# Performance work log

Hardware: AMD Instinct MI355X
Metric: run time of the kernel (lower is better)

## Reference

```python
import jax, jax.numpy as jnp
import numpy as np

B, CIN, H, W = 2, 8, 224, 224
P, S, K, WIN = 10, 5, 7, 3      # patchsize, stride, k neighbours, window radius = 15 // stride
E, F = 8, 64                    # embedding out-channels, cnn hidden features
N1 = (H - P) // S + 1
N2 = (W - P) // S + 1
N = N1 * N2                     # patches per image (43*43 = 1849)


def _conv(x, w, b):
    y = jax.lax.conv_general_dilated(x, w, (1, 1), 'SAME',
                                     dimension_numbers=('NCHW', 'OIHW', 'NCHW'))
    return y + b[None, :, None, None]


def _cnn3(x, w1, b1, w2, b2, w3, b3):
    # conv-relu, conv-relu, conv (depth=3, bn disabled)
    h = jax.nn.relu(_conv(x, w1, b1))
    h = jax.nn.relu(_conv(h, w2, b2))
    return _conv(h, w3, b3)


def _patches(x):
    # x: [B,C,H,W] -> [B, N, C*P*P] (im2col with stride S)
    ri = jnp.arange(N1)[:, None] * S + jnp.arange(P)[None, :]   # [N1,P]
    ci = jnp.arange(N2)[:, None] * S + jnp.arange(P)[None, :]   # [N2,P]
    p = x[:, :, ri, :][..., ci]            # [B,C,N1,P,N2,P]
    p = p.transpose(0, 2, 4, 1, 3, 5)      # [B,N1,N2,C,P,P]
    return p.reshape(x.shape[0], N, -1)


def _candidates():
    q1, q2 = jnp.meshgrid(jnp.arange(N1), jnp.arange(N2), indexing='ij')
    off = jnp.arange(-WIN, WIN + 1)
    c1 = jnp.clip(q1[..., None, None] + off[:, None], 0, N1 - 1)   # [N1,N2,7,7]
    c2 = jnp.clip(q2[..., None, None] + off[None, :], 0, N2 - 1)
    return (c1 * N2 + c2).reshape(N, -1)   # [N, m], m=49


def _fold(pats, C):
    # pats: [B,N,C*P*P] -> [B,C,H,W], overlap-add then normalize by counts
    pats = pats.reshape(B, N, C, P, P).transpose(0, 2, 1, 3, 4).reshape(B, C, -1)
    rr = jnp.arange(N1)[:, None] * S + jnp.arange(P)[None, :]
    cc = jnp.arange(N2)[:, None] * S + jnp.arange(P)[None, :]
    R = jnp.broadcast_to(rr[:, None, :, None], (N1, N2, P, P)).reshape(-1)
    Cc = jnp.broadcast_to(cc[None, :, None, :], (N1, N2, P, P)).reshape(-1)
    out = jnp.zeros((B, C, H, W), pats.dtype).at[:, :, R, Cc].add(pats)
    cnt = jnp.zeros((H, W), pats.dtype).at[R, Cc].add(1.0)
    return out / jnp.maximum(cnt, 1.0)


def setup_inputs() -> dict:
    key = jax.random.key(0)
    ks = jax.random.split(key, 8)
    sd = 0.05
    d = {"x": jax.random.normal(ks[0], (B, CIN, H, W), jnp.float32)}
    # embedding cnn: CIN->F->F->E
    d["w1e"] = jax.random.normal(ks[1], (F, CIN, 3, 3), jnp.float32) * sd
    d["b1e"] = jnp.zeros((F,), jnp.float32)
    d["w2e"] = jax.random.normal(ks[2], (F, F, 3, 3), jnp.float32) * sd
    d["b2e"] = jnp.zeros((F,), jnp.float32)
    d["w3e"] = jax.random.normal(ks[3], (E, F, 3, 3), jnp.float32) * sd
    d["b3e"] = jnp.zeros((E,), jnp.float32)
    # temperature cnn: CIN->F->F->1
    d["w1t"] = jax.random.normal(ks[4], (F, CIN, 3, 3), jnp.float32) * sd
    d["b1t"] = jnp.zeros((F,), jnp.float32)
    d["w2t"] = jax.random.normal(ks[5], (F, F, 3, 3), jnp.float32) * sd
    d["b2t"] = jnp.zeros((F,), jnp.float32)
    d["w3t"] = jax.random.normal(ks[6], (1, F, 3, 3), jnp.float32) * sd
    d["b3t"] = jnp.zeros((1,), jnp.float32)
    return d


def reference(x, w1e, b1e, w2e, b2e, w3e, b3e, w1t, b1t, w2t, b2t, w3t, b3t):
    xe = _cnn3(x, w1e, b1e, w2e, b2e, w3e, b3e)           # [B,E,H,W] patch embedding
    log_temp = _cnn3(x, w1t, b1t, w2t, b2t, w3t, b3t)     # [B,1,H,W] log temperature

    pe = _patches(xe)                                     # [B,N,E*P*P]
    yp = _patches(x)                                      # [B,N,CIN*P*P]
    lt = _patches(log_temp).mean(-1)                      # [B,N] per-patch log temp
    idx = _candidates()                                   # [N,m]

    # negative squared euclidean distance, gathered at window candidates
    sq = jnp.sum(pe * pe, -1)                             # [B,N]
    G = jnp.einsum('bnd,bmd->bnm', pe, pe)                # [B,N,N] patch Gram
    Dfull = -(sq[:, :, None] + sq[:, None, :] - 2.0 * G)
    Dc = Dfull[:, jnp.arange(N)[:, None], idx]            # [B,N,m]

    self_mask = (idx == jnp.arange(N)[:, None])[None]     # exclude_self=True
    logits = Dc * jnp.exp(-lt)[..., None]                 # temperature-scaled
    logits = jnp.where(self_mask, -1e9, logits)

    # continuous (neural) k-nearest-neighbour weights
    ws, cur = [], logits
    for _ in range(K):
        w = jax.nn.softmax(cur, axis=-1)
        ws.append(w)
        cur = cur + jnp.log1p(-jnp.minimum(w, 1.0 - 1e-6))
    Wk = jnp.stack(ws, axis=-1)                           # [B,N,m,K]

    yg = yp[:, idx]                                       # [B,N,m,dy] gathered neighbour patches
    nb = jnp.einsum('bnmk,bnmd->kbnd', Wk, yg)            # [K,B,N,dy]
    vols = [_fold(nb[j], CIN) for j in range(K)]
    return jnp.concatenate([x] + vols, axis=1)            # [B,(K+1)*CIN,H,W]
```

## Files before the change

kernel.cpp:

```cpp
#include <hip/hip_runtime.h>
#include <math.h>

namespace {
constexpr int B_ = 2, CIN = 8, H_ = 224, W_ = 224;
constexpr int K_ = 7;
constexpr int F_ = 64, E_ = 8;
constexpr int N1 = 43, N2 = 43, N_ = N1 * N2;
constexpr int M_ = 49;
constexpr int D_ = 800;
constexpr int HW = H_ * W_;

constexpr size_t FHW = (size_t)B_ * F_ * HW;
constexpr size_t OFF_H1E = 0;
constexpr size_t OFF_H1T = OFF_H1E + FHW;
constexpr size_t OFF_H2E = OFF_H1T + FHW;
constexpr size_t OFF_H2T = OFF_H2E + FHW;
constexpr size_t OFF_WK  = 0;
constexpr size_t OFF_XE  = OFF_H2T + FHW;
constexpr size_t OFF_LTM = OFF_XE + (size_t)B_ * E_ * HW;
constexpr size_t OFF_PE  = OFF_LTM + (size_t)B_ * HW;
constexpr size_t OFF_LT  = OFF_PE + (size_t)B_ * N_ * D_;
constexpr size_t OFF_SQ  = OFF_LT + (size_t)B_ * N_;
constexpr int WPREP_N = 294912;
constexpr int WPREP1_N = 12288;
constexpr int WPREP3_N = 9216;
constexpr int WPREP_TOT = WPREP_N + WPREP1_N + 2 * WPREP3_N;

__device__ __forceinline__ int clampi(int v, int lo, int hi) {
  return min(max(v, lo), hi);
}

__device__ __forceinline__ int xcd_swz(int x, int nwg) {
  int xcd = x & 7, idx = x >> 3;
  int q = nwg >> 3, r = nwg & 7;
  int base = (xcd < r) ? xcd * (q + 1) : r * (q + 1) + (xcd - r) * q;
  return base + idx;
}

typedef __attribute__((ext_vector_type(8))) short short8;
typedef __attribute__((ext_vector_type(4))) float float4v;
typedef __attribute__((ext_vector_type(4))) unsigned short ushort4v;
}

__global__ __launch_bounds__(256) void wprep_k(
    const float* __restrict__ w_e, const float* __restrict__ w_t,
    const float* __restrict__ w1e, const float* __restrict__ w1t,
    const float* __restrict__ w3e, const float* __restrict__ w3t,
    unsigned short* __restrict__ whi, unsigned short* __restrict__ wlo,
    unsigned short* __restrict__ whi1, unsigned short* __restrict__ wlo1,
    unsigned short* __restrict__ whi3, unsigned short* __restrict__ wlo3) {
  int t = blockIdx.x * 256 + threadIdx.x;
  if (t >= WPREP_TOT) return;
  float v;
  unsigned short* dh;
  unsigned short* dl;
  int di;
  if (t < WPREP_N) {
    int j = t & 7;
    int lane = (t >> 3) & 63;
    int wv = (t >> 9) & 3;
    int t2 = t >> 11;
    int idx = t2 % 9;
    int t3 = t2 / 9;
    int kcb = t3 & 1;
    int br = t3 >> 1;
    const float* wgt = br ? w_t : w_e;
    int co = wv * 16 + (lane & 15);
    int ci = kcb * 32 + 8 * (lane >> 4) + j;
    v = wgt[((size_t)co * 64 + ci) * 9 + idx];
    dh = whi; dl = wlo; di = t;
  } else if (t < WPREP_N + WPREP1_N) {
    int t1 = t - WPREP_N;
    int j = t1 & 7;
    int lane = (t1 >> 3) & 63;
    int wv = (t1 >> 9) & 3;
    int t2 = t1 >> 11;
    int ky = t2 % 3;
    int br = t2 / 3;
    const float* wgt = br ? w1t : w1e;
    int co = wv * 16 + (lane & 15);
    int kx = lane >> 4;
    int ci = j;
    v = (kx < 3) ? wgt[(((size_t)co * 8 + ci) * 3 + ky) * 3 + kx] : 0.f;
    dh = whi1; dl = wlo1; di = t1;
  } else {
    int t3v = t - WPREP_N - WPREP1_N;
    int set = t3v / WPREP3_N;
    int rem = t3v - set * WPREP3_N;
    int j = rem & 7;
    int lane = (rem >> 3) & 63;
    int t2 = rem >> 9;
    int idx = t2 % 9;
    int kcb = t2 / 9;
    int co = lane & 15;
    int ci = kcb * 32 + 8 * (lane >> 4) + j;
    if (set == 0)
      v = (co < 8) ? w3e[((size_t)co * 64 + ci) * 9 + idx] : 0.f;
    else
      v = (co == 0) ? w3t[(size_t)ci * 9 + idx] : 0.f;
    dh = whi3; dl = wlo3; di = t3v;
  }
  unsigned u = __float_as_uint(v);
  unsigned short hi = (unsigned short)(u >> 16);
  float rem = v - __uint_as_float(u & 0xffff0000u);
  unsigned short lo = (unsigned short)(__float_as_uint(rem) >> 16);
  dh[di] = hi;
  dl[di] = lo;
}

__global__ __launch_bounds__(256) void conv1_k(
    const float* __restrict__ x,
    const unsigned short* __restrict__ whi1, const unsigned short* __restrict__ wlo1,
    const float* __restrict__ b_e, float* __restrict__ o_e,
    const float* __restrict__ b_t, float* __restrict__ o_t) {
  const int tile = blockIdx.x;
  const int b = blockIdx.z & 1;
  const int br = blockIdx.z >> 1;
  const float* bias = br ? b_t : b_e;
  float* out = br ? o_t : o_e;

  const int th0 = (tile / 14) * 16, tw0 = (tile % 14) * 16;
  const int tid = threadIdx.x;
  const int wv = tid >> 6, lane = tid & 63;
  const int q = lane >> 4, n = lane & 15;

  __shared__ unsigned short sT[342 * 20];

  const float* xB = x + (size_t)b * CIN * HW;
#pragma unroll
  for (int it = 0; it < 2; ++it) {
    int s = tid + 256 * it;
    if (s < 342) {
      int lr = s / 19, lc = s - lr * 19;
      int gh = th0 + lr - 1, gw = tw0 + lc - 1;
      short8 h8, l8;
#pragma unroll
      for (int ci = 0; ci < 8; ++ci) { h8[ci] = 0; l8[ci] = 0; }
      if (lc < 18 && gh >= 0 && gh < H_ && gw >= 0 && gw < W_) {
        const float* xp = xB + (size_t)gh * W_ + gw;
#pragma unroll
        for (int ci = 0; ci < 8; ++ci) {
          float v = xp[(size_t)ci * HW];
          unsigned u = __float_as_uint(v);
          float rem = v - __uint_as_float(u & 0xffff0000u);
          h8[ci] = (short)(u >> 16);
          l8[ci] = (short)(__float_as_uint(rem) >> 16);
        }
      }
      *(short8*)&sT[s * 20] = h8;
      *(short8*)&sT[s * 20 + 8] = l8;
    }
  }

  const short8* wh8 = (const short8*)whi1;
  const short8* wl8 = (const short8*)wlo1;
  short8 Ah[3], Al[3];
#pragma unroll
  for (int ky = 0; ky < 3; ++ky) {
    int ab = ((br * 3 + ky) * 4 + wv) * 64 + lane;
    Ah[ky] = wh8[ab];
    Al[ky] = wl8[ab];
  }

  float4v acc[16];
#pragma unroll
  for (int pr = 0; pr < 16; ++pr) acc[pr] = (float4v)0.f;

  __syncthreads();

#pragma unroll
  for (int r = 0; r < 18; ++r) {
    const unsigned short* p = &sT[(r * 19 + n + q) * 20];
    short8 Bh = *(const short8*)p;
    short8 Bl = *(const short8*)(p + 8);
#pragma unroll
    for (int ky = 0; ky < 3; ++ky) {
      const int pr = r - ky;
      if (pr >= 0 && pr < 16) {
        acc[pr] = __builtin_amdgcn_mfma_f32_16x16x32_bf16(Ah[ky], Bh, acc[pr], 0, 0, 0);
        acc[pr] = __builtin_amdgcn_mfma_f32_16x16x32_bf16(Al[ky], Bh, acc[pr], 0, 0, 0);
        acc[pr] = __builtin_amdgcn_mfma_f32_16x16x32_bf16(Ah[ky], Bl, acc[pr], 0, 0, 0);
      }
    }
  }

  float4v bv = *(const float4v*)&bias[wv * 16 + 4 * q];
#pragma unroll
  for (int pr = 0; pr < 16; ++pr) {
    float4v v;
#pragma unroll
    for (int r = 0; r < 4; ++r) v[r] = fmaxf(acc[pr][r] + bv[r], 0.f);
    *(float4v*)&out[(((size_t)b * H_ + th0 + pr) * W_ + tw0 + n) * 64 + wv * 16 + 4 * q] = v;
  }
}

__global__ __launch_bounds__(256) void conv2_mfma_k(
    const float* __restrict__ in_e, const float* __restrict__ in_t,
    const unsigned short* __restrict__ whi, const unsigned short* __restrict__ wlo,
    const float* __restrict__ b_e, const float* __restrict__ b_t,
    unsigned short* __restrict__ ehi, unsigned short* __restrict__ elo,
    unsigned short* __restrict__ thi, unsigned short* __restrict__ tlo) {
  constexpr int NLD = 21;
  const int tile = blockIdx.x;
  const int b = blockIdx.z & 1;
  const int br = blockIdx.z >> 1;
  const float* in = br ? in_t : in_e;
  const float* bias = br ? b_t : b_e;
  unsigned short* ohi = br ? thi : ehi;
  unsigned short* olo = br ? tlo : elo;

  const int th0 = (tile / 14) * 16, tw0 = (tile % 14) * 16;
  const int tid = threadIdx.x;
  const int wv = tid >> 6, lane = tid & 63;
  const int q = lane >> 4, n = lane & 15;

  __shared__ unsigned short sT[18 * 18 * 72];
  unsigned* sT32 = (unsigned*)sT;

  float4v acc[16];
#pragma unroll
  for (int pr = 0; pr < 16; ++pr) acc[pr] = (float4v)0.f;

  const float* inB = in + (size_t)b * HW * 64;
  const short8* whi8 = (const short8*)whi;
  const short8* wlo8 = (const short8*)wlo;

  int po[NLD];
  unsigned okm = 0;
#pragma unroll
  for (int j = 0; j < NLD; ++j) {
    int s = tid + 256 * j;
    int sp = s >> 4, cp = s & 15;
    int lr = sp / 18, lc = sp - lr * 18;
    int gh = th0 + lr - 1, gw = tw0 + lc - 1;
    bool ok = (s < 5184) && gh >= 0 && gh < H_ && gw >= 0 && gw < W_;
    po[j] = ok ? (gh * W_ + gw) * 64 + 2 * cp : 0;
    if (ok) okm |= (1u << j);
  }

  for (int kcb = 0; kcb < 2; ++kcb) {
    float2 stg[NLD];
#pragma unroll
    for (int j = 0; j < NLD; ++j)
      stg[j] = *(const float2*)&inB[(size_t)po[j] + kcb * 32];

    __syncthreads();
#pragma unroll
    for (int j = 0; j < NLD; ++j) {
      int s = tid + 256 * j;
      if (s < 5184) {
        int sp = s >> 4, cp = s & 15;
        bool ok = (okm >> j) & 1;
        float vx = ok ? stg[j].x : 0.f;
        float vy = ok ? stg[j].y : 0.f;
        unsigned u0 = __float_as_uint(vx), u1 = __float_as_uint(vy);
        float r0 = vx - __uint_as_float(u0 & 0xffff0000u);
        float r1 = vy - __uint_as_float(u1 & 0xffff0000u);
        unsigned l0 = __float_as_uint(r0) >> 16, l1 = __float_as_uint(r1) >> 16;
        sT32[sp * 36 + cp] = (u0 >> 16) | ((u1 >> 16) << 16);
        sT32[sp * 36 + 16 + cp] = l0 | (l1 << 16);
      }
    }
    __syncthreads();

    short8 Ah[9], Al[9];
    const int abase = (((br * 2 + kcb) * 9) * 4 + wv) * 64 + lane;
#pragma unroll
    for (int idx = 0; idx < 9; ++idx) {
      Ah[idx] = whi8[abase + idx * 256];
      Al[idx] = wlo8[abase + idx * 256];
    }

#pragma unroll
    for (int r = 0; r < 18; ++r) {
      short8 Bh[3], Bl[3];
#pragma unroll
      for (int kx = 0; kx < 3; ++kx) {
        const unsigned short* p = &sT[(r * 18 + n + kx) * 72 + 8 * q];
        Bh[kx] = *(const short8*)p;
        Bl[kx] = *(const short8*)(p + 32);
      }
#pragma unroll
      for (int ky = 0; ky < 3; ++ky) {
        const int pr = r - ky;
        if (pr >= 0 && pr < 16) {
#pragma unroll
          for (int kx = 0; kx < 3; ++kx) {
            const int idx = ky * 3 + kx;
            acc[pr] = __builtin_amdgcn_mfma_f32_16x16x32_bf16(Ah[idx], Bh[kx], acc[pr], 0, 0, 0);
            acc[pr] = __builtin_amdgcn_mfma_f32_16x16x32_bf16(Al[idx], Bh[kx], acc[pr], 0, 0, 0);
            acc[pr] = __builtin_amdgcn_mfma_f32_16x16x32_bf16(Ah[idx], Bl[kx], acc[pr], 0, 0, 0);
          }
        }
      }
    }
  }

  float4v bv = *(const float4v*)&bias[wv * 16 + 4 * q];
  unsigned short* sHi = (unsigned short*)sT;
  unsigned short* sLo = sHi + 128 * 68;
  __syncthreads();
#pragma unroll
  for (int hf = 0; hf < 2; ++hf) {
#pragma unroll
    for (int pr8 = 0; pr8 < 8; ++pr8) {
      int pr = hf * 8 + pr8;
      int px = pr8 * 16 + n;
      ushort4v hv, lv;
#pragma unroll
      for (int r = 0; r < 4; ++r) {
        float v = fmaxf(acc[pr][r] + bv[r], 0.f);
        unsigned u = __float_as_uint(v);
        float rem = v - __uint_as_float(u & 0xffff0000u);
        hv[r] = (unsigned short)(u >> 16);
        lv[r] = (unsigned short)(__float_as_uint(rem) >> 16);
      }
      *(ushort4v*)&sHi[px * 68 + wv * 16 + 4 * q] = hv;
      *(ushort4v*)&sLo[px * 68 + wv * 16 + 4 * q] = lv;
    }
    __syncthreads();
#pragma unroll
    for (int i = 0; i < 4; ++i) {
      int f = tid + 256 * i;
      int px = f >> 3, c8 = f & 7;
      int h = th0 + hf * 8 + (px >> 4), w = tw0 + (px & 15);
      size_t o = ((size_t)(b * H_ + h) * W_ + w) * 64 + c8 * 8;
      *(short8*)&ohi[o] = *(const short8*)&sHi[px * 68 + c8 * 8];
      *(short8*)&olo[o] = *(const short8*)&sLo[px * 68 + c8 * 8];
    }
    __syncthreads();
  }
}

__global__ __launch_bounds__(256) void conv3_mfma_k(
    const unsigned short* __restrict__ h2ehi, const unsigned short* __restrict__ h2elo,
    const unsigned short* __restrict__ h2thi, const unsigned short* __restrict__ h2tlo,
    const unsigned short* __restrict__ whi3, const unsigned short* __restrict__ wlo3,
    const float* __restrict__ b3e, const float* __restrict__ b3t,
    float* __restrict__ xe, float* __restrict__ ltm) {
  constexpr int NLD = 12;
  const int tile = blockIdx.x;
  const int b = blockIdx.z & 1;
  const int br = blockIdx.z >> 1;
  const unsigned short* ihi = (br ? h2thi : h2ehi) + (size_t)b * HW * 64;
  const unsigned short* ilo = (br ? h2tlo : h2elo) + (size_t)b * HW * 64;

  const int th0 = (tile / 14) * 8, tw0 = (tile % 14) * 16;
  const int tid = threadIdx.x;
  const int wv = tid >> 6, lane = tid & 63;
  const int q = lane >> 4, n = lane & 15;

  __shared__ unsigned short sT[180 * 72];
  unsigned* sT32 = (unsigned*)sT;

  int po[NLD];
  unsigned okm = 0;
#pragma unroll
  for (int j = 0; j < NLD; ++j) {
    int s = tid + 256 * j;
    int sp = s >> 4, cp = s & 15;
    int lr = sp / 18, lc = sp - lr * 18;
    int gh = th0 + lr - 1, gw = tw0 + lc - 1;
    bool ok = (s < 2880) && gh >= 0 && gh < H_ && gw >= 0 && gw < W_;
    po[j] = ok ? (gh * W_ + gw) * 64 + 2 * cp : 0;
    if (ok) okm |= (1u << j);
  }

  const short8* wh8 = (const short8*)whi3;
  const short8* wl8 = (const short8*)wlo3;
  const int brBase = br * 1152;

  float4v acc[2];
  acc[0] = (float4v)0.f;
  acc[1] = (float4v)0.f;

  for (int kcb = 0; kcb < 2; ++kcb) {
    unsigned sgh[NLD], sgl[NLD];
#pragma unroll
    for (int j = 0; j < NLD; ++j) {
      sgh[j] = *(const unsigned*)&ihi[(size_t)po[j] + kcb * 32];
      sgl[j] = *(const unsigned*)&ilo[(size_t)po[j] + kcb * 32];
    }
    __syncthreads();
#pragma unroll
    for (int j = 0; j < NLD; ++j) {
      int s = tid + 256 * j;
      if (s < 2880) {
        int sp = s >> 4, cp = s & 15;
        bool ok = (okm >> j) & 1;
        sT32[sp * 36 + cp] = ok ? sgh[j] : 0u;
        sT32[sp * 36 + 16 + cp] = ok ? sgl[j] : 0u;
      }
    }
    __syncthreads();

    short8 Ah[9], Al[9];
#pragma unroll
    for (int idx = 0; idx < 9; ++idx) {
      int fe = brBase + (kcb * 9 + idx) * 64 + lane;
      Ah[idx] = wh8[fe];
      Al[idx] = wl8[fe];
    }

#pragma unroll
    for (int r = 0; r < 4; ++r) {
      const int rr = 2 * wv + r;
      short8 Bh[3], Bl[3];
#pragma unroll
      for (int kx = 0; kx < 3; ++kx) {
        const unsigned short* p = &sT[(rr * 18 + n + kx) * 72 + 8 * q];
        Bh[kx] = *(const short8*)p;
        Bl[kx] = *(const short8*)(p + 32);
      }
#pragma unroll
      for (int ky = 0; ky < 3; ++ky) {
        const int pl = r - ky;
        if (pl >= 0 && pl < 2) {
#pragma unroll
          for (int kx = 0; kx < 3; ++kx) {
            const int idx = ky * 3 + kx;
            acc[pl] = __builtin_amdgcn_mfma_f32_16x16x32_bf16(Ah[idx], Bh[kx], acc[pl], 0, 0, 0);
            acc[pl] = __builtin_amdgcn_mfma_f32_16x16x32_bf16(Al[idx], Bh[kx], acc[pl], 0, 0, 0);
            acc[pl] = __builtin_amdgcn_mfma_f32_16x16x32_bf16(Ah[idx], Bl[kx], acc[pl], 0, 0, 0);
          }
        }
      }
    }
  }

  if (br == 0) {
    if (q < 2) {
      float4v bv = *(const float4v*)&b3e[4 * q];
#pragma unroll
      for (int pl = 0; pl < 2; ++pl) {
        int h = th0 + 2 * wv + pl;
#pragma unroll
        for (int r = 0; r < 4; ++r)
          xe[((size_t)(b * 8 + 4 * q + r) * H_ + h) * W_ + tw0 + n] = acc[pl][r] + bv[r];
      }
    }
  } else {
    if (q == 0) {
      float bt = b3t[0];
#pragma unroll
      for (int pl = 0; pl < 2; ++pl) {
        int h = th0 + 2 * wv + pl;
        ltm[(size_t)b * HW + h * W_ + tw0 + n] = acc[pl][0] + bt;
      }
    }
  }
}

__global__ __launch_bounds__(256) void prep_k(const float* __restrict__ xe,
                                              const float* __restrict__ ltm,
                                              float* __restrict__ pe,
                                              float* __restrict__ lt,
                                              float* __restrict__ sq) {
  const int n = blockIdx.x, b = blockIdx.y;
  const int tid = threadIdx.x;
  const int wv = tid >> 6, lane = tid & 63;
  const int q1 = n / N2, q2 = n % N2;
  const int r0 = q1 * 5, c0 = q2 * 5;

  float s = 0.f;
  float* peR = pe + ((size_t)b * N_ + n) * D_;
#pragma unroll
  for (int j = 0; j < 4; ++j) {
    int d = tid + 256 * j;
    if (d < D_) {
      int c = d / 100;
      int rr = (d / 10) % 10;
      int cc = d % 10;
      size_t si = ((size_t)(b * 8 + c) * H_ + r0 + rr) * W_ + c0 + cc;
      float ve = xe[si];
      peR[d] = ve;
      s += ve * ve;
    }
  }
  float t = 0.f;
  if (tid < 100) t = ltm[(size_t)b * HW + (r0 + tid / 10) * W_ + c0 + tid % 10];

#pragma unroll
  for (int off = 32; off > 0; off >>= 1) {
    s += __shfl_xor(s, off);
    t += __shfl_xor(t, off);
  }
  __shared__ float rs[4], rt[4];
  if (lane == 0) { rs[wv] = s; rt[wv] = t; }
  __syncthreads();
  if (tid == 0) {
    sq[b * N_ + n] = rs[0] + rs[1] + rs[2] + rs[3];
    lt[b * N_ + n] = (rt[0] + rt[1] + rt[2] + rt[3]) * 0.01f;
  }
}

__global__ __launch_bounds__(256) void attn_w_k(const float* __restrict__ pe,
                                                const float* __restrict__ lt,
                                                const float* __restrict__ sq,
                                                float* __restrict__ wk) {
  const int wv = threadIdx.x >> 6, lane = threadIdx.x & 63;
  const int ng = xcd_swz(blockIdx.x, (N_ + 3) / 4);
  const int n = ng * 4 + wv;
  if (n >= N_) return;
  const int b = blockIdx.y;
  const int q1 = n / N2, q2 = n % N2;

  const float* peB = pe + (size_t)b * N_ * D_;
  const float* qrow = peB + (size_t)n * D_;
  float q[13];
#pragma unroll
  for (int t = 0; t < 13; ++t) {
    int s = t * 64 + lane;
    q[t] = (s < D_) ? qrow[s] : 0.f;
  }

  const float sqn = sq[b * N_ + n];
  const float itemp = expf(-lt[b * N_ + n]);
  float gm = -INFINITY;

  for (int o1 = 0; o1 < 7; ++o1) {
    int c1 = clampi(q1 + o1 - 3, 0, N1 - 1);
    const float* rowb = peB + (size_t)(c1 * N2) * D_;
#pragma unroll
    for (int o2 = 0; o2 < 7; ++o2) {
      int c2 = clampi(q2 + o2 - 3, 0, N2 - 1);
      int cn = c1 * N2 + c2;
      const float* crow = rowb + (size_t)c2 * D_;
      float a = 0.f;
#pragma unroll
      for (int t = 0; t < 13; ++t) {
        float v;
        if (t < 12) v = crow[t * 64 + lane];
        else v = (lane < 32) ? crow[768 + lane] : 0.f;
        a += q[t] * v;
      }
#pragma unroll
      for (int off = 32; off > 0; off >>= 1) a += __shfl_xor(a, off);
      float Dv = -(sqn + sq[b * N_ + cn] - 2.f * a);
      float lg = (cn == n) ? -1e9f : Dv * itemp;
      const int m = o1 * 7 + o2;
      gm = (lane == m) ? lg : gm;
    }
  }

  float cur = (lane < M_) ? gm : -INFINITY;
  float* wrow = wk + (size_t)(b * N_ + n) * (M_ * K_);
#pragma unroll
  for (int k = 0; k < K_; ++k) {
    float mx = cur;
#pragma unroll
    for (int off = 32; off > 0; off >>= 1) mx = fmaxf(mx, __shfl_xor(mx, off));
    float e = (lane < M_) ? expf(cur - mx) : 0.f;
    float ssum = e;
#pragma unroll
    for (int off = 32; off > 0; off >>= 1) ssum += __shfl_xor(ssum, off);
    float w = e / ssum;
    if (lane < M_) wrow[lane * K_ + k] = w;
    cur += log1pf(-fminf(w, 1.f - 1e-6f));
  }
}

__global__ __launch_bounds__(256) void foldpv_k(const float* __restrict__ x,
                                                const float* __restrict__ wk,
                                                float* __restrict__ out) {
  int i = blockIdx.x * 256 + threadIdx.x;
  if (i >= B_ * HW) return;
  const int w = i % W_;
  const int h = (i / W_) % H_;
  const int b = i / HW;
  const int c0 = blockIdx.z * 4;

  const float* xB = x + (size_t)b * CIN * HW;
  const int pix = h * W_ + w;
  float* outB = out + (size_t)b * 64 * HW + pix;

#pragma unroll
  for (int c = 0; c < 4; ++c)
    outB[(size_t)(c0 + c) * HW] = xB[(size_t)(c0 + c) * HW + pix];

  const int q1lo = max(0, (h - 5) / 5), q1hi = min(N1 - 1, h / 5);
  const int q2lo = max(0, (w - 5) / 5), q2hi = min(N2 - 1, w / 5);

  float acc[4][7];
#pragma unroll
  for (int c = 0; c < 4; ++c)
#pragma unroll
    for (int k = 0; k < 7; ++k) acc[c][k] = 0.f;

  int cnt = 0;
  for (int q1 = q1lo; q1 <= q1hi; ++q1) {
    const int ib = h - 5 * q1;
    for (int q2 = q2lo; q2 <= q2hi; ++q2) {
      ++cnt;
      const int jb = w - 5 * q2;
      const int n = q1 * N2 + q2;
      const float* wrow = wk + (size_t)(b * N_ + n) * (M_ * K_);
#pragma unroll
      for (int o1 = 0; o1 < 7; ++o1) {
        const int c1 = clampi(q1 + o1 - 3, 0, N1 - 1);
        const int row = c1 * 5 + ib;
#pragma unroll
        for (int o2 = 0; o2 < 7; ++o2) {
          const int c2 = clampi(q2 + o2 - 3, 0, N2 - 1);
          const int col = c2 * 5 + jb;
          const float* xp = xB + (size_t)c0 * HW + (size_t)row * W_ + col;
          float xv[4];
#pragma unroll
          for (int c = 0; c < 4; ++c) xv[c] = xp[(size_t)c * HW];
          const float* wp = wrow + (o1 * 7 + o2) * 7;
          float wm[7];
#pragma unroll
          for (int k = 0; k < 7; ++k) wm[k] = wp[k];
#pragma unroll
          for (int c = 0; c < 4; ++c)
#pragma unroll
            for (int k = 0; k < 7; ++k) acc[c][k] += wm[k] * xv[c];
        }
      }
    }
  }

  const float inv = (cnt > 0) ? 1.f / (float)cnt : 0.f;
#pragma unroll
  for (int k = 0; k < 7; ++k)
#pragma unroll
    for (int c = 0; c < 4; ++c)
      outB[(size_t)(8 + k * 8 + c0 + c) * HW] = acc[c][k] * inv;
}

extern "C" void kernel_launch(void* const* d_in, const int* in_sizes, int n_in,
                              void* d_out, int out_size, void* d_ws,
                              size_t ws_size, hipStream_t stream) {
  const float* x   = (const float*)d_in[0];
  const float* w1e = (const float*)d_in[1];
  const float* b1e = (const float*)d_in[2];
  const float* w2e = (const float*)d_in[3];
  const float* b2e = (const float*)d_in[4];
  const float* w3e = (const float*)d_in[5];
  const float* b3e = (const float*)d_in[6];
  const float* w1t = (const float*)d_in[7];
  const float* b1t = (const float*)d_in[8];
  const float* w2t = (const float*)d_in[9];
  const float* b2t = (const float*)d_in[10];
  const float* w3t = (const float*)d_in[11];
  const float* b3t = (const float*)d_in[12];

  float* ws  = (float*)d_ws;
  float* out = (float*)d_out;

  float* h1e = ws + OFF_H1E;
  float* h1t = ws + OFF_H1T;
  unsigned short* h2ehi = (unsigned short*)(ws + OFF_H2E);
  unsigned short* h2elo = h2ehi + (size_t)B_ * HW * 64;
  unsigned short* h2thi = (unsigned short*)(ws + OFF_H2T);
  unsigned short* h2tlo = h2thi + (size_t)B_ * HW * 64;
  float* wkb = ws + OFF_WK;
  float* xe  = ws + OFF_XE;
  float* ltm = ws + OFF_LTM;
  float* pe  = ws + OFF_PE;
  float* lt  = ws + OFF_LT;
  float* sqv = ws + OFF_SQ;
  unsigned short* whi  = (unsigned short*)(ws + OFF_XE);
  unsigned short* wlo  = whi + WPREP_N;
  unsigned short* whi1 = wlo + WPREP_N;
  unsigned short* wlo1 = whi1 + WPREP1_N;
  unsigned short* whi3 = (unsigned short*)(ws + OFF_PE);
  unsigned short* wlo3 = whi3 + 2 * WPREP3_N;

  wprep_k<<<(WPREP_TOT + 255) / 256, 256, 0, stream>>>(
      w2e, w2t, w1e, w1t, w3e, w3t, whi, wlo, whi1, wlo1, whi3, wlo3);
  conv1_k<<<dim3(196, 1, 4), 256, 0, stream>>>(x, whi1, wlo1, b1e, h1e, b1t, h1t);
  conv2_mfma_k<<<dim3(196, 1, 4), 256, 0, stream>>>(h1e, h1t, whi, wlo, b2e, b2t,
                                                    h2ehi, h2elo, h2thi, h2tlo);
  conv3_mfma_k<<<dim3(392, 1, 4), 256, 0, stream>>>(h2ehi, h2elo, h2thi, h2tlo,
                                                    whi3, wlo3, b3e, b3t, xe, ltm);
  prep_k<<<dim3(N_, B_), 256, 0, stream>>>(xe, ltm, pe, lt, sqv);
  attn_w_k<<<dim3((N_ + 3) / 4, B_), 256, 0, stream>>>(pe, lt, sqv, wkb);
  foldpv_k<<<dim3((B_ * HW + 255) / 256, 1, 2), 256, 0, stream>>>(x, wkb, out);
}
```

Measured before the change: 332.8 us.

## Tile foldpv into 16x16 blocks with LDS-staged weights and channel-last input

Adds a kernel that transposes the input x into a channel-last copy, so the fold kernel can fetch 4 channels with one vector load. The fold kernel now works on 16x16 pixel tiles with XCD-swizzled block ids. It stages the neighbour weights for all patches covering the tile into shared memory, padded from 7 to 8 entries so they can be read as vectors. This replaces redundant per-thread global loads of weights and strided channel loads, at the cost of an extra transpose kernel, about 39KB of LDS per block, and reuse of the h1t workspace region.

Result: faster. 301.4 us (-9.4%).

```diff
diff --git a/kernel.cpp b/kernel.cpp
--- a/kernel.cpp
+++ b/kernel.cpp
@@ -16,6 +16,7 @@
 constexpr size_t OFF_H2E = OFF_H1T + FHW;
 constexpr size_t OFF_H2T = OFF_H2E + FHW;
 constexpr size_t OFF_WK  = 0;
+constexpr size_t OFF_XCL = OFF_H1T;
 constexpr size_t OFF_XE  = OFF_H2T + FHW;
 constexpr size_t OFF_LTM = OFF_XE + (size_t)B_ * E_ * HW;
 constexpr size_t OFF_PE  = OFF_LTM + (size_t)B_ * HW;
@@ -39,6 +40,7 @@
 
 typedef __attribute__((ext_vector_type(8))) short short8;
 typedef __attribute__((ext_vector_type(4))) float float4v;
+typedef __attribute__((ext_vector_type(2))) float float2v;
 typedef __attribute__((ext_vector_type(4))) unsigned short ushort4v;
 }
 
@@ -451,6 +453,21 @@
   }
 }
 
+__global__ __launch_bounds__(256) void xcl_k(const float* __restrict__ x,
+                                             float* __restrict__ xcl) {
+  int i = blockIdx.x * 256 + threadIdx.x;
+  if (i >= B_ * HW) return;
+  int b = i / HW, pix = i % HW;
+  const float* xp = x + (size_t)b * CIN * HW + pix;
+  float4v v0, v1;
+#pragma unroll
+  for (int c = 0; c < 4; ++c) v0[c] = xp[(size_t)c * HW];
+#pragma unroll
+  for (int c = 0; c < 4; ++c) v1[c] = xp[(size_t)(4 + c) * HW];
+  *(float4v*)&xcl[(size_t)i * 8] = v0;
+  *(float4v*)&xcl[(size_t)i * 8 + 4] = v1;
+}
+
 __global__ __launch_bounds__(256) void prep_k(const float* __restrict__ xe,
                                               const float* __restrict__ ltm,
                                               float* __restrict__ pe,
@@ -560,23 +577,41 @@
   }
 }
 
-__global__ __launch_bounds__(256) void foldpv_k(const float* __restrict__ x,
+__global__ __launch_bounds__(256) void foldpv_k(const float* __restrict__ xcl,
                                                 const float* __restrict__ wk,
                                                 float* __restrict__ out) {
-  int i = blockIdx.x * 256 + threadIdx.x;
-  if (i >= B_ * HW) return;
-  const int w = i % W_;
-  const int h = (i / W_) % H_;
-  const int b = i / HW;
+  const int tile = xcd_swz(blockIdx.x, 196);
+  const int b = blockIdx.y;
   const int c0 = blockIdx.z * 4;
-
-  const float* xB = x + (size_t)b * CIN * HW;
+  const int ty0 = (tile / 14) * 16, tx0 = (tile % 14) * 16;
+  const int tid = threadIdx.x;
+  const int h = ty0 + (tid >> 4), w = tx0 + (tid & 15);
+
+  const int q1lo_t = max(0, (ty0 - 5) / 5), q1hi_t = min(N1 - 1, (ty0 + 15) / 5);
+  const int q2lo_t = max(0, (tx0 - 5) / 5), q2hi_t = min(N2 - 1, (tx0 + 15) / 5);
+  const int nq1 = q1hi_t - q1lo_t + 1, nq2 = q2hi_t - q2lo_t + 1;
+
+  __shared__ float sWk[25 * 392];
+  {
+    const int tot = nq1 * nq2 * 392;
+    for (int s = tid; s < tot; s += 256) {
+      int lq = s / 392, r = s - lq * 392;
+      int m = r >> 3, k = r & 7;
+      int n = (q1lo_t + lq / nq2) * N2 + (q2lo_t + lq % nq2);
+      sWk[s] = (k < 7) ? wk[(size_t)(b * N_ + n) * (M_ * K_) + m * 7 + k] : 0.f;
+    }
+  }
+  __syncthreads();
+
+  const float* xclB = xcl + (size_t)b * HW * 8;
   const int pix = h * W_ + w;
   float* outB = out + (size_t)b * 64 * HW + pix;
 
-#pragma unroll
-  for (int c = 0; c < 4; ++c)
-    outB[(size_t)(c0 + c) * HW] = xB[(size_t)(c0 + c) * HW + pix];
+  {
+    float4v pv = *(const float4v*)&xclB[(size_t)pix * 8 + c0];
+#pragma unroll
+    for (int c = 0; c < 4; ++c) outB[(size_t)(c0 + c) * HW] = pv[c];
+  }
 
   const int q1lo = max(0, (h - 5) / 5), q1hi = min(N1 - 1, h / 5);
   const int q2lo = max(0, (w - 5) / 5), q2hi = min(N2 - 1, w / 5);
@@ -590,11 +625,11 @@
   int cnt = 0;
   for (int q1 = q1lo; q1 <= q1hi; ++q1) {
     const int ib = h - 5 * q1;
+    const int lq1 = q1 - q1lo_t;
     for (int q2 = q2lo; q2 <= q2hi; ++q2) {
       ++cnt;
       const int jb = w - 5 * q2;
-      const int n = q1 * N2 + q2;
-      const float* wrow = wk + (size_t)(b * N_ + n) * (M_ * K_);
+      const float* wq = sWk + (lq1 * nq2 + (q2 - q2lo_t)) * 392;
 #pragma unroll
       for (int o1 = 0; o1 < 7; ++o1) {
         const int c1 = clampi(q1 + o1 - 3, 0, N1 - 1);
@@ -603,18 +638,21 @@
         for (int o2 = 0; o2 < 7; ++o2) {
           const int c2 = clampi(q2 + o2 - 3, 0, N2 - 1);
           const int col = c2 * 5 + jb;
-          const float* xp = xB + (size_t)c0 * HW + (size_t)row * W_ + col;
-          float xv[4];
-#pragma unroll
-          for (int c = 0; c < 4; ++c) xv[c] = xp[(size_t)c * HW];
-          const float* wp = wrow + (o1 * 7 + o2) * 7;
-          float wm[7];
-#pragma unroll
-          for (int k = 0; k < 7; ++k) wm[k] = wp[k];
-#pragma unroll
-          for (int c = 0; c < 4; ++c)
-#pragma unroll
-            for (int k = 0; k < 7; ++k) acc[c][k] += wm[k] * xv[c];
+          float4v xv = *(const float4v*)&xclB[((size_t)row * W_ + col) * 8 + c0];
+          const float* wp = wq + (o1 * 7 + o2) * 8;
+          float4v w4 = *(const float4v*)wp;
+          float2v w2 = *(const float2v*)(wp + 4);
+          float w6 = wp[6];
+#pragma unroll
+          for (int c = 0; c < 4; ++c) {
+            acc[c][0] += w4[0] * xv[c];
+            acc[c][1] += w4[1] * xv[c];
+            acc[c][2] += w4[2] * xv[c];
+            acc[c][3] += w4[3] * xv[c];
+            acc[c][4] += w2[0] * xv[c];
+            acc[c][5] += w2[1] * xv[c];
+            acc[c][6] += w6 * xv[c];
+          }
         }
       }
     }
@@ -666,15 +704,17 @@
   unsigned short* wlo1 = whi1 + WPREP1_N;
   unsigned short* whi3 = (unsigned short*)(ws + OFF_PE);
   unsigned short* wlo3 = whi3 + 2 * WPREP3_N;
+  float* xcl = ws + OFF_XCL;
 
   wprep_k<<<(WPREP_TOT + 255) / 256, 256, 0, stream>>>(
       w2e, w2t, w1e, w1t, w3e, w3t, whi, wlo, whi1, wlo1, whi3, wlo3);
   conv1_k<<<dim3(196, 1, 4), 256, 0, stream>>>(x, whi1, wlo1, b1e, h1e, b1t, h1t);
   conv2_mfma_k<<<dim3(196, 1, 4), 256, 0, stream>>>(h1e, h1t, whi, wlo, b2e, b2t,
                                                     h2ehi, h2elo, h2thi, h2tlo);
+  xcl_k<<<(B_ * HW + 255) / 256, 256, 0, stream>>>(x, xcl);
   conv3_mfma_k<<<dim3(392, 1, 4), 256, 0, stream>>>(h2ehi, h2elo, h2thi, h2tlo,
                                                     whi3, wlo3, b3e, b3t, xe, ltm);
   prep_k<<<dim3(N_, B_), 256, 0, stream>>>(xe, ltm, pe, lt, sqv);
   attn_w_k<<<dim3((N_ + 3) / 4, B_), 256, 0, stream>>>(pe, lt, sqv, wkb);
-  foldpv_k<<<dim3((B_ * HW + 255) / 256, 1, 2), 256, 0, stream>>>(x, wkb, out);
-}
+  foldpv_k<<<dim3(196, B_, 2), 256, 0, stream>>>(xcl, wkb, out);
+}
```
